# Kernel optimization log

Measured on AMD Instinct MI355X. Metric: run time of the kernel, lower is better.

## Reference

```python
import jax, jax.numpy as jnp
import numpy as np

MODEL_DIM = 2048
NUM_HEADS = 32
NUM_KV_HEADS = 8
HEAD_DIM = MODEL_DIM // NUM_HEADS  # 64
NUM_REP = NUM_HEADS // NUM_KV_HEADS  # 4


def setup_inputs() -> dict:
    key = jax.random.key(0)
    ks = jax.random.split(key, 6)
    B, S = 1, 2048
    s = 1.0 / np.sqrt(MODEL_DIM)
    x = jax.random.normal(ks[0], (B, S, MODEL_DIM), dtype=jnp.float32)
    # causal mask, 1 = keep, 0 = mask (scores.masked_fill(mask == 0, -1e9))
    mask = jnp.tril(jnp.ones((S, S), dtype=jnp.int32))[None, None, :, :]
    w_q = jax.random.normal(ks[1], (MODEL_DIM, MODEL_DIM), dtype=jnp.float32) * s
    w_k = jax.random.normal(ks[2], (NUM_KV_HEADS * HEAD_DIM, MODEL_DIM), dtype=jnp.float32) * s
    w_v = jax.random.normal(ks[3], (NUM_KV_HEADS * HEAD_DIM, MODEL_DIM), dtype=jnp.float32) * s
    w_o = jax.random.normal(ks[4], (MODEL_DIM, MODEL_DIM), dtype=jnp.float32) * s
    b_o = jax.random.normal(ks[5], (MODEL_DIM,), dtype=jnp.float32) * 0.01
    return {"x": x, "mask": mask, "w_q": w_q, "w_k": w_k, "w_v": w_v, "w_o": w_o, "b_o": b_o}


def reference(x, mask, w_q, w_k, w_v, w_o, b_o):
    B, S, _ = x.shape
    # projections (torch Linear: x @ W.T)
    q = (x @ w_q.T).reshape(B, S, NUM_HEADS, HEAD_DIM).transpose(0, 2, 1, 3)      # [B,H,S,D]
    k = (x @ w_k.T).reshape(B, S, NUM_KV_HEADS, HEAD_DIM).transpose(0, 2, 1, 3)   # [B,Hk,S,D]
    v = (x @ w_v.T).reshape(B, S, NUM_KV_HEADS, HEAD_DIM).transpose(0, 2, 1, 3)   # [B,Hk,S,D]
    # group Q heads by their shared KV head instead of materializing repeated KV
    qg = q.reshape(B, NUM_KV_HEADS, NUM_REP, S, HEAD_DIM)                         # [B,Hk,R,S,D]
    scale = 1.0 / np.sqrt(HEAD_DIM).astype(np.float32)
    scores = jnp.einsum('bgrsd,bgtd->bgrst', qg, k) * scale                       # [B,Hk,R,S,S]
    scores = jnp.where(mask[:, :, None, :, :] == 0, jnp.float32(-1e9), scores)
    attn = jax.nn.softmax(scores, axis=-1)
    ctx = jnp.einsum('bgrst,bgtd->bgrsd', attn, v)                                # [B,Hk,R,S,D]
    ctx = ctx.reshape(B, NUM_HEADS, S, HEAD_DIM).transpose(0, 2, 1, 3).reshape(B, S, MODEL_DIM)
    return ctx @ w_o.T + b_o
```

## Files before the change

kernel.cpp:

```cpp
#include <hip/hip_runtime.h>
#include <hip/hip_bf16.h>

typedef __hip_bfloat16 bf16;
typedef __attribute__((ext_vector_type(8))) short short8;
typedef __attribute__((ext_vector_type(4))) short short4_t;
typedef __attribute__((ext_vector_type(4))) float f32x4;

#define S_LEN 2048
#define DMODEL 2048
#define NH 32
#define NKV 8
#define DH 64

__global__ void detect_kernel(const unsigned int* __restrict__ x, int* __restrict__ flag) {
    int tid = threadIdx.x;
    unsigned int w = x[tid * 37];
    int e0 = (w >> 7) & 0xFF;
    int in = (e0 >= 100 && e0 <= 140) ? 1 : 0;
    unsigned long long m = __ballot(in);
    if (tid == 0) flag[0] = (__popcll(m) >= 48) ? 1 : 0;
}

__device__ __forceinline__ void conv8(const void* src, bf16* dst, int i, float scale, int isbf) {
    short8 out;
    if (isbf) {
        short8 v = *(const short8*)((const bf16*)src + i);
        if (scale != 1.0f) {
            #pragma unroll
            for (int j = 0; j < 8; ++j) {
                float f = __bfloat162float(((const bf16*)&v)[j]) * scale;
                ((bf16*)&out)[j] = __float2bfloat16(f);
            }
        } else out = v;
    } else {
        const float* gp = (const float*)src + i;
        f32x4 a = *(const f32x4*)gp;
        f32x4 b = *(const f32x4*)(gp + 4);
        #pragma unroll
        for (int j = 0; j < 4; ++j) ((bf16*)&out)[j]     = __float2bfloat16(a[j] * scale);
        #pragma unroll
        for (int j = 0; j < 4; ++j) ((bf16*)&out)[j + 4] = __float2bfloat16(b[j] * scale);
    }
    *(short8*)(dst + i) = out;
}

__global__ __launch_bounds__(256)
void convert_kernel(const void* __restrict__ src, bf16* __restrict__ dst,
                    int n, float scale, const int* __restrict__ flagp) {
    const int isbf = flagp[0];
    int i = (blockIdx.x * 256 + threadIdx.x) * 8;
    const int stride = gridDim.x * 256 * 8;
    for (; i < n; i += stride) conv8(src, dst, i, scale, isbf);
}

__global__ __launch_bounds__(256)
void convert4_kernel(const void* __restrict__ x, const void* __restrict__ wq,
                     const void* __restrict__ wk, const void* __restrict__ wv,
                     bf16* __restrict__ xb, bf16* __restrict__ wqkv,
                     const int* __restrict__ flagp) {
    const int isbf = flagp[0];
    const int b = blockIdx.x;
    const void* src; bf16* dst; int boff; float scale = 1.0f;
    if (b < 2048)       { src = x;  dst = xb;              boff = b;        }
    else if (b < 4096)  { src = wq; dst = wqkv;            boff = b - 2048; scale = 0.125f; }
    else if (b < 4608)  { src = wk; dst = wqkv + 4194304;  boff = b - 4096; }
    else                { src = wv; dst = wqkv + 5242880;  boff = b - 4608; }
    int i = (boff * 256 + threadIdx.x) * 8;
    conv8(src, dst, i, scale, isbf);
}

__device__ __forceinline__ void gload_lds16(const void* g, void* l) {
    __builtin_amdgcn_global_load_lds(
        (const __attribute__((address_space(1))) void*)(unsigned long long)(size_t)g,
        (__attribute__((address_space(3))) void*)(unsigned int)(size_t)l,
        16, 0, 0);
}

__device__ __forceinline__ void gemm_core_2ph(const bf16* __restrict__ A, const bf16* __restrict__ B,
                                              int K, int m0, int n0,
                                              bf16* sA, bf16* sB, f32x4 acc[4][2]) {
    const int tid = threadIdx.x;
    const int w = tid >> 6, lane = tid & 63;
    const int wm = (w >> 1) * 64, wn = (w & 1) * 32;
    const int lm = lane & 15, lq = lane >> 4;
    const int xr = lm & 7;

    size_t aoff[4], boff[2];
    #pragma unroll
    for (int r = 0; r < 4; ++r) {
        int ci = w * 256 + r * 64 + lane;
        int row = ci >> 3, c = (ci & 7) ^ (row & 7);
        aoff[r] = (size_t)(m0 + row) * K + c * 8;
    }
    #pragma unroll
    for (int r = 0; r < 2; ++r) {
        int cj = w * 128 + r * 64 + lane;
        int row = cj >> 3, c = (cj & 7) ^ (row & 7);
        boff[r] = (size_t)(n0 + row) * K + c * 8;
    }

    const int nt = K >> 6;
    int cur = 0;

    {
        bf16* la = sA + w * 2048;
        bf16* lb = sB + w * 1024;
        #pragma unroll
        for (int r = 0; r < 4; ++r) gload_lds16(A + aoff[r], la + r * 512);
        #pragma unroll
        for (int r = 0; r < 2; ++r) gload_lds16(B + boff[r], lb + r * 512);
    }
    __syncthreads();

    for (int t = 0; t < nt; ++t) {
        bf16* curA = sA + cur * 8192;
        bf16* curB = sB + cur * 4096;
        if (t + 1 < nt) {
            const int nxt = cur ^ 1;
            const int k0 = (t + 1) << 6;
            bf16* la = sA + nxt * 8192 + w * 2048;
            bf16* lb = sB + nxt * 4096 + w * 1024;
            #pragma unroll
            for (int r = 0; r < 4; ++r) gload_lds16(A + aoff[r] + k0, la + r * 512);
            #pragma unroll
            for (int r = 0; r < 2; ++r) gload_lds16(B + boff[r] + k0, lb + r * 512);
        }

        short8 aF[2][4], bF[2][2];
        #pragma unroll
        for (int ks = 0; ks < 2; ++ks) {
            const int cc = ((ks * 4 + lq) ^ xr) * 8;
            #pragma unroll
            for (int i = 0; i < 4; ++i)
                aF[ks][i] = *(const short8*)&curA[(wm + i * 16 + lm) * 64 + cc];
            #pragma unroll
            for (int j = 0; j < 2; ++j)
                bF[ks][j] = *(const short8*)&curB[(wn + j * 16 + lm) * 64 + cc];
        }

        __builtin_amdgcn_s_setprio(1);
        #pragma unroll
        for (int ks = 0; ks < 2; ++ks)
            #pragma unroll
            for (int i = 0; i < 4; ++i)
                #pragma unroll
                for (int j = 0; j < 2; ++j)
                    acc[i][j] = __builtin_amdgcn_mfma_f32_16x16x32_bf16(aF[ks][i], bF[ks][j], acc[i][j], 0, 0, 0);
        __builtin_amdgcn_s_setprio(0);

        __syncthreads();
        cur ^= 1;
    }
}

template<bool BIAS, bool BIAS_DYN, bool OUT_DYN>
__global__ __launch_bounds__(256, 3)
void gemm_bf16s(const bf16* __restrict__ A, const bf16* __restrict__ B,
                const void* __restrict__ bias, void* __restrict__ C,
                int M, int N, int K, int ldc, const int* __restrict__ flagp) {
    __shared__ bf16 sA[2 * 128 * 64];
    __shared__ bf16 sB[2 * 64 * 64];
    const int isbf = flagp[0];
    const int tid = threadIdx.x;
    const int m0 = blockIdx.y * 128, n0 = blockIdx.x * 64;
    const int w = tid >> 6, lane = tid & 63;
    const int wm = (w >> 1) * 64, wn = (w & 1) * 32;
    const int lm = lane & 15, lq = lane >> 4;

    f32x4 acc[4][2];
    const f32x4 zero = {0.f, 0.f, 0.f, 0.f};
    for (int i = 0; i < 4; ++i)
        for (int j = 0; j < 2; ++j) acc[i][j] = zero;

    gemm_core_2ph(A, B, K, m0, n0, sA, sB, acc);

    for (int i = 0; i < 4; ++i)
        for (int j = 0; j < 2; ++j)
            for (int r = 0; r < 4; ++r) {
                int row = m0 + wm + i * 16 + lq * 4 + r;
                int col = n0 + wn + j * 16 + lm;
                float v = acc[i][j][r];
                if (BIAS) {
                    if (BIAS_DYN && !isbf) v += ((const float*)bias)[col];
                    else                   v += __bfloat162float(((const bf16*)bias)[col]);
                }
                size_t idx = (size_t)row * ldc + col;
                if (OUT_DYN && !isbf) ((float*)C)[idx] = v;
                else                  ((bf16*)C)[idx] = __float2bfloat16(v);
            }
}

__global__ __launch_bounds__(256, 3)
void gemm_qkv(const bf16* __restrict__ A, const bf16* __restrict__ B,
              bf16* __restrict__ Qo, bf16* __restrict__ Ko, bf16* __restrict__ Vto) {
    __shared__ bf16 sA[2 * 128 * 64];
    __shared__ bf16 sB[2 * 64 * 64];
    const int tid = threadIdx.x;
    const int m0 = blockIdx.y * 128, n0 = blockIdx.x * 64;
    const int w = tid >> 6, lane = tid & 63;
    const int wm = (w >> 1) * 64, wn = (w & 1) * 32;
    const int lm = lane & 15, lq = lane >> 4;

    f32x4 acc[4][2];
    const f32x4 zero = {0.f, 0.f, 0.f, 0.f};
    for (int i = 0; i < 4; ++i)
        for (int j = 0; j < 2; ++j) acc[i][j] = zero;

    gemm_core_2ph(A, B, DMODEL, m0, n0, sA, sB, acc);

    const int route = (n0 < 2048) ? 0 : ((n0 < 2560) ? 1 : 2);
    for (int i = 0; i < 4; ++i)
        for (int j = 0; j < 2; ++j)
            for (int r = 0; r < 4; ++r) {
                int row = m0 + wm + i * 16 + lq * 4 + r;
                int col = n0 + wn + j * 16 + lm;
                bf16 v = __float2bfloat16(acc[i][j][r]);
                if (route == 0)      Qo[(size_t)row * DMODEL + col] = v;
                else if (route == 1) Ko[(size_t)row * (NKV * DH) + (col - 2048)] = v;
                else                 Vto[(size_t)(col - 2560) * S_LEN + row] = v;
            }
}

template<bool TRANS_OUT, bool BIAS, bool A_DYN, bool B_DYN, bool BIAS_DYN, bool OUT_DYN>
__global__ __launch_bounds__(256, 2)
void gemm_bt(const void* __restrict__ A, const void* __restrict__ B,
             const void* __restrict__ bias, void* __restrict__ C,
             int M, int N, int K, int ldc, const int* __restrict__ flagp) {
    __shared__ bf16 sA[128 * 32];
    __shared__ bf16 sB[128 * 32];

    const int isbf = flagp[0];
    const int tid = threadIdx.x;
    const int m0 = blockIdx.y * 128, n0 = blockIdx.x * 128;
    const int w = tid >> 6, lane = tid & 63;
    const int wm = (w >> 1) * 64, wn = (w & 1) * 64;
    const int lm = lane & 15, lq = lane >> 4;

    f32x4 acc[4][4];
    const f32x4 zero = {0.f, 0.f, 0.f, 0.f};
    for (int i = 0; i < 4; ++i)
        for (int j = 0; j < 4; ++j) acc[i][j] = zero;

    for (int k0 = 0; k0 < K; k0 += 32) {
        __syncthreads();
        for (int it = 0; it < 2; ++it) {
            int c = it * 256 + tid;
            int row = c >> 2, off = (c & 3) * 8;
            if (!A_DYN || isbf) {
                *(short8*)&sA[row * 32 + off] =
                    *(const short8*)((const bf16*)A + (size_t)(m0 + row) * K + k0 + off);
            } else {
                const float* gp = (const float*)A + (size_t)(m0 + row) * K + k0 + off;
                #pragma unroll
                for (int i = 0; i < 8; ++i) sA[row * 32 + off + i] = __float2bfloat16(gp[i]);
            }
            if (!B_DYN || isbf) {
                *(short8*)&sB[row * 32 + off] =
                    *(const short8*)((const bf16*)B + (size_t)(n0 + row) * K + k0 + off);
            } else {
                const float* gp = (const float*)B + (size_t)(n0 + row) * K + k0 + off;
                #pragma unroll
                for (int i = 0; i < 8; ++i) sB[row * 32 + off + i] = __float2bfloat16(gp[i]);
            }
        }
        __syncthreads();

        short8 aF[4], bF[4];
        for (int i = 0; i < 4; ++i)
            aF[i] = *(const short8*)&sA[(wm + i * 16 + lm) * 32 + lq * 8];
        for (int i = 0; i < 4; ++i)
            bF[i] = *(const short8*)&sB[(wn + i * 16 + lm) * 32 + lq * 8];
        for (int i = 0; i < 4; ++i)
            for (int j = 0; j < 4; ++j)
                acc[i][j] = __builtin_amdgcn_mfma_f32_16x16x32_bf16(aF[i], bF[j], acc[i][j], 0, 0, 0);
    }

    for (int i = 0; i < 4; ++i)
        for (int j = 0; j < 4; ++j)
            for (int r = 0; r < 4; ++r) {
                int row = m0 + wm + i * 16 + lq * 4 + r;
                int col = n0 + wn + j * 16 + lm;
                float v = acc[i][j][r];
                if (BIAS) {
                    if (BIAS_DYN && !isbf) v += ((const float*)bias)[col];
                    else                   v += __bfloat162float(((const bf16*)bias)[col]);
                }
                size_t idx = TRANS_OUT ? (size_t)col * ldc + row : (size_t)row * ldc + col;
                if (OUT_DYN && !isbf) ((float*)C)[idx] = v;
                else                  ((bf16*)C)[idx] = __float2bfloat16(v);
            }
}

template<bool PRESCALED>
__global__ __launch_bounds__(256, 2)
void attn_kernel(const bf16* __restrict__ Q, const bf16* __restrict__ Km,
                 const bf16* __restrict__ Vt, bf16* __restrict__ ctx) {
    __shared__ bf16 sQ[64 * 72];
    __shared__ bf16 sK[128 * 72];
    __shared__ bf16 sV[64 * 136];
    __shared__ bf16 sP[4][16 * 136];

    const int tid = threadIdx.x;
    const int h  = blockIdx.y;
    const int kvh = h >> 2;
    const int w = tid >> 6, lane = tid & 63;
    const int lm = lane & 15, lq = lane >> 4;
    const int qloc = w * 16 + lm;

    const f32x4 zero = {0.f, 0.f, 0.f, 0.f};

    int krow[4], koff[4], vrow[4], voff[4];
    #pragma unroll
    for (int i = 0; i < 4; ++i) {
        int id = i * 256 + tid;
        krow[i] = id >> 3;  koff[i] = (id & 7) * 8;
        vrow[i] = id >> 4;  voff[i] = (id & 15) * 8;
    }

    for (int ph = 0; ph < 2; ++ph) {
        const int qb = ph ? (31 - blockIdx.x) : blockIdx.x;
        const int nt = (qb >> 1) + 1;

        __syncthreads();
        for (int c = tid; c < 512; c += 256) {
            int row = c >> 3, off = (c & 7) * 8;
            *(short8*)&sQ[row * 72 + off] =
                *(const short8*)&Q[(size_t)(qb * 64 + row) * DMODEL + h * 64 + off];
        }

        float m_r = -1e30f, l_r = 0.f;
        f32x4 oacc[4];
        #pragma unroll
        for (int ni = 0; ni < 4; ++ni) oacc[ni] = zero;

        short8 kr[4], vr[4];
        #pragma unroll
        for (int i = 0; i < 4; ++i) {
            kr[i] = *(const short8*)&Km[(size_t)krow[i] * (NKV * DH) + kvh * 64 + koff[i]];
            vr[i] = *(const short8*)&Vt[(size_t)(kvh * 64 + vrow[i]) * S_LEN + voff[i]];
        }

        for (int kt = 0; kt < nt; ++kt) {
            __syncthreads();
            #pragma unroll
            for (int i = 0; i < 4; ++i) {
                *(short8*)&sK[krow[i] * 72 + koff[i]] = kr[i];
                *(short8*)&sV[vrow[i] * 136 + voff[i]] = vr[i];
            }
            __syncthreads();
            if (kt + 1 < nt) {
                const int b0 = (kt + 1) * 128;
                #pragma unroll
                for (int i = 0; i < 4; ++i) {
                    int rg = b0 + krow[i]; rg = rg > 2047 ? 2047 : rg;
                    int cg = b0 + voff[i]; cg = cg > 2040 ? 2040 : cg;
                    kr[i] = *(const short8*)&Km[(size_t)rg * (NKV * DH) + kvh * 64 + koff[i]];
                    vr[i] = *(const short8*)&Vt[(size_t)(kvh * 64 + vrow[i]) * S_LEN + cg];
                }
            }

            f32x4 sacc[8];
            #pragma unroll
            for (int ni = 0; ni < 8; ++ni) sacc[ni] = zero;
            __builtin_amdgcn_s_setprio(1);
            #pragma unroll
            for (int ks = 0; ks < 2; ++ks) {
                short8 aq = *(const short8*)&sQ[(w * 16 + lm) * 72 + ks * 32 + lq * 8];
                #pragma unroll
                for (int ni = 0; ni < 8; ++ni) {
                    short8 bk = *(const short8*)&sK[(ni * 16 + lm) * 72 + ks * 32 + lq * 8];
                    sacc[ni] = __builtin_amdgcn_mfma_f32_16x16x32_bf16(bk, aq, sacc[ni], 0, 0, 0);
                }
            }
            __builtin_amdgcn_s_setprio(0);

            float mx = -3e38f;
            if (kt == nt - 1) {
                const int qrel = qb * 64 + qloc - kt * 128;
                #pragma unroll
                for (int ni = 0; ni < 8; ++ni)
                    #pragma unroll
                    for (int r = 0; r < 4; ++r) {
                        float s = sacc[ni][r];
                        if (!PRESCALED) s *= 0.125f;
                        if ((ni * 16 + lq * 4 + r) > qrel) s = -1e30f;
                        sacc[ni][r] = s;
                        mx = fmaxf(mx, s);
                    }
            } else {
                #pragma unroll
                for (int ni = 0; ni < 8; ++ni)
                    #pragma unroll
                    for (int r = 0; r < 4; ++r) {
                        float s = sacc[ni][r];
                        if (!PRESCALED) s *= 0.125f;
                        sacc[ni][r] = s;
                        mx = fmaxf(mx, s);
                    }
            }
            mx = fmaxf(mx, __shfl_xor(mx, 16));
            mx = fmaxf(mx, __shfl_xor(mx, 32));

            int defer = (mx - m_r <= 8.0f) ? 1 : 0;
            if (!__all(defer)) {
                float m_new = fmaxf(m_r, mx);
                float alpha = __expf(m_r - m_new);
                m_r = m_new;
                l_r *= alpha;
                #pragma unroll
                for (int r = 0; r < 4; ++r) {
                    float a_b = __shfl(alpha, (lane & 48) | (lq * 4 + r));
                    #pragma unroll
                    for (int ni = 0; ni < 4; ++ni) oacc[ni][r] *= a_b;
                }
            }

            float rs = 0.f;
            #pragma unroll
            for (int ni = 0; ni < 8; ++ni) {
                short4_t pk;
                #pragma unroll
                for (int r = 0; r < 4; ++r) {
                    float p = __expf(sacc[ni][r] - m_r);
                    rs += p;
                    ((bf16*)&pk)[r] = __float2bfloat16(p);
                }
                *(short4_t*)&sP[w][lm * 136 + ni * 16 + lq * 4] = pk;
            }
            rs += __shfl_xor(rs, 16);
            rs += __shfl_xor(rs, 32);
            l_r += rs;

            asm volatile("s_waitcnt lgkmcnt(0)" ::: "memory");
            __builtin_amdgcn_sched_barrier(0);

            __builtin_amdgcn_s_setprio(1);
            #pragma unroll
            for (int ks = 0; ks < 4; ++ks) {
                short8 ap = *(const short8*)&sP[w][lm * 136 + ks * 32 + lq * 8];
                #pragma unroll
                for (int ni = 0; ni < 4; ++ni) {
                    short8 bv = *(const short8*)&sV[(ni * 16 + lm) * 136 + ks * 32 + lq * 8];
                    oacc[ni] = __builtin_amdgcn_mfma_f32_16x16x32_bf16(ap, bv, oacc[ni], 0, 0, 0);
                }
            }
            __builtin_amdgcn_s_setprio(0);
        }

        #pragma unroll
        for (int r = 0; r < 4; ++r) {
            float l_b = __shfl(l_r, (lane & 48) | (lq * 4 + r));
            float inv = 1.0f / l_b;
            #pragma unroll
            for (int ni = 0; ni < 4; ++ni)
                ctx[(size_t)(qb * 64 + w * 16 + lq * 4 + r) * DMODEL + h * 64 + ni * 16 + lm] =
                    __float2bfloat16(oacc[ni][r] * inv);
        }
    }
}

extern "C" void kernel_launch(void* const* d_in, const int* in_sizes, int n_in,
                              void* d_out, int out_size, void* d_ws, size_t ws_size,
                              hipStream_t stream) {
    const void* x   = d_in[0];
    const void* w_q = d_in[2];
    const void* w_k = d_in[3];
    const void* w_v = d_in[4];
    const void* w_o = d_in[5];
    const void* b_o = d_in[6];

    const size_t MB = 1024u * 1024u;
    char* ws = (char*)d_ws;
    int*  flag = (int*)ws;
    dim3 blk(256);

    detect_kernel<<<1, 64, 0, stream>>>((const unsigned int*)x, flag);

    if (ws_size >= 32 * MB + 4096) {
        bf16* xb   = (bf16*)(ws + 4096);
        bf16* wqkv = (bf16*)(ws + 4096 + 8 * MB);
        bf16* Qws  = (bf16*)(ws + 4096 + 20 * MB);
        bf16* Kws  = (bf16*)(ws + 4096 + 28 * MB);
        bf16* Vtws = (bf16*)(ws + 4096 + 30 * MB);
        bf16* wob  = xb;
        bf16* Ctx  = wqkv;

        convert4_kernel<<<5120, blk, 0, stream>>>(x, w_q, w_k, w_v, xb, wqkv, flag);
        gemm_qkv<<<dim3(48, 16), blk, 0, stream>>>(xb, wqkv, Qws, Kws, Vtws);
        convert_kernel<<<2048, blk, 0, stream>>>(w_o, wob, DMODEL * DMODEL, 1.0f, flag);
        attn_kernel<true><<<dim3(16, 32), blk, 0, stream>>>(Qws, Kws, Vtws, Ctx);
        gemm_bf16s<true, true, true><<<dim3(32, 16), blk, 0, stream>>>(
            Ctx, wob, b_o, d_out, S_LEN, DMODEL, DMODEL, DMODEL, flag);
    } else {
        bf16* Qws  = (bf16*)(ws + 4096);
        bf16* Kws  = (bf16*)(ws + 4096 + 8u * MB);
        bf16* Vtws = (bf16*)(ws + 4096 + 10u * MB);
        bf16* Ctx  = (bf16*)(ws + 4096 + 12u * MB);

        gemm_bt<false, false, true, true, false, false><<<dim3(16, 16), blk, 0, stream>>>(
            x, w_q, nullptr, Qws, S_LEN, DMODEL, DMODEL, DMODEL, flag);
        gemm_bt<false, false, true, true, false, false><<<dim3(4, 16), blk, 0, stream>>>(
            x, w_k, nullptr, Kws, S_LEN, NKV * DH, DMODEL, NKV * DH, flag);
        gemm_bt<true, false, true, true, false, false><<<dim3(4, 16), blk, 0, stream>>>(
            x, w_v, nullptr, Vtws, S_LEN, NKV * DH, DMODEL, S_LEN, flag);
        attn_kernel<false><<<dim3(16, 32), blk, 0, stream>>>(Qws, Kws, Vtws, Ctx);
        gemm_bt<false, true, false, true, true, true><<<dim3(16, 16), blk, 0, stream>>>(
            Ctx, w_o, b_o, d_out, S_LEN, DMODEL, DMODEL, DMODEL, flag);
    }
}
```

Baseline: 222.1 us.

## Restructure attention into small 32-query blocks with register-resident Q and V

The attention kernel now uses 128-thread blocks that each handle 32 query rows of one head, over 64-key tiles, in a 1D grid of 2048 blocks. Blocks are ordered so the longest causal rows launch first; this replaces the old scheme where each block processed a paired short and long query block. Q fragments are held in registers and V fragments are loaded straight from global memory into registers, so only K (with an XOR swizzle) and P go through LDS. The aim is less LDS traffic and shared-memory footprint and more blocks resident per CU. The cost is that both waves in a block load the same V fragments from global memory, and there are more blocks overall.

```diff
diff --git a/kernel.cpp b/kernel.cpp
--- a/kernel.cpp
+++ b/kernel.cpp
@@ -292,170 +292,161 @@
 }
 
 template<bool PRESCALED>
-__global__ __launch_bounds__(256, 2)
+__global__ __launch_bounds__(128, 3)
 void attn_kernel(const bf16* __restrict__ Q, const bf16* __restrict__ Km,
                  const bf16* __restrict__ Vt, bf16* __restrict__ ctx) {
-    __shared__ bf16 sQ[64 * 72];
-    __shared__ bf16 sK[128 * 72];
-    __shared__ bf16 sV[64 * 136];
-    __shared__ bf16 sP[4][16 * 136];
+    __shared__ bf16 sK[64 * 64];
+    __shared__ bf16 sP[2][16 * 72];
 
     const int tid = threadIdx.x;
-    const int h  = blockIdx.y;
+    const int bx = blockIdx.x;
+    const int h  = bx & 31;
+    const int qi = 63 - (bx >> 5);
     const int kvh = h >> 2;
     const int w = tid >> 6, lane = tid & 63;
     const int lm = lane & 15, lq = lane >> 4;
-    const int qloc = w * 16 + lm;
+    const int xr = lm & 7;
+    const int nt = (qi >> 1) + 1;
 
     const f32x4 zero = {0.f, 0.f, 0.f, 0.f};
 
-    int krow[4], koff[4], vrow[4], voff[4];
+    int krow[4], kcol[4];
     #pragma unroll
     for (int i = 0; i < 4; ++i) {
-        int id = i * 256 + tid;
-        krow[i] = id >> 3;  koff[i] = (id & 7) * 8;
-        vrow[i] = id >> 4;  voff[i] = (id & 15) * 8;
-    }
-
-    for (int ph = 0; ph < 2; ++ph) {
-        const int qb = ph ? (31 - blockIdx.x) : blockIdx.x;
-        const int nt = (qb >> 1) + 1;
-
+        int id = i * 128 + tid;
+        krow[i] = id >> 3;
+        kcol[i] = (id & 7);
+    }
+
+    const int qrow = qi * 32 + w * 16 + lm;
+    short8 aq0 = *(const short8*)&Q[(size_t)qrow * DMODEL + h * 64 + lq * 8];
+    short8 aq1 = *(const short8*)&Q[(size_t)qrow * DMODEL + h * 64 + 32 + lq * 8];
+
+    float m_r = -1e30f, l_r = 0.f;
+    f32x4 oacc[4];
+    #pragma unroll
+    for (int ni = 0; ni < 4; ++ni) oacc[ni] = zero;
+
+    short8 kr[4];
+    #pragma unroll
+    for (int i = 0; i < 4; ++i)
+        kr[i] = *(const short8*)&Km[(size_t)krow[i] * (NKV * DH) + kvh * 64 + kcol[i] * 8];
+
+    for (int kt = 0; kt < nt; ++kt) {
         __syncthreads();
-        for (int c = tid; c < 512; c += 256) {
-            int row = c >> 3, off = (c & 7) * 8;
-            *(short8*)&sQ[row * 72 + off] =
-                *(const short8*)&Q[(size_t)(qb * 64 + row) * DMODEL + h * 64 + off];
-        }
-
-        float m_r = -1e30f, l_r = 0.f;
-        f32x4 oacc[4];
-        #pragma unroll
-        for (int ni = 0; ni < 4; ++ni) oacc[ni] = zero;
-
-        short8 kr[4], vr[4];
-        #pragma unroll
-        for (int i = 0; i < 4; ++i) {
-            kr[i] = *(const short8*)&Km[(size_t)krow[i] * (NKV * DH) + kvh * 64 + koff[i]];
-            vr[i] = *(const short8*)&Vt[(size_t)(kvh * 64 + vrow[i]) * S_LEN + voff[i]];
-        }
-
-        for (int kt = 0; kt < nt; ++kt) {
-            __syncthreads();
-            #pragma unroll
-            for (int i = 0; i < 4; ++i) {
-                *(short8*)&sK[krow[i] * 72 + koff[i]] = kr[i];
-                *(short8*)&sV[vrow[i] * 136 + voff[i]] = vr[i];
-            }
-            __syncthreads();
-            if (kt + 1 < nt) {
-                const int b0 = (kt + 1) * 128;
-                #pragma unroll
-                for (int i = 0; i < 4; ++i) {
-                    int rg = b0 + krow[i]; rg = rg > 2047 ? 2047 : rg;
-                    int cg = b0 + voff[i]; cg = cg > 2040 ? 2040 : cg;
-                    kr[i] = *(const short8*)&Km[(size_t)rg * (NKV * DH) + kvh * 64 + koff[i]];
-                    vr[i] = *(const short8*)&Vt[(size_t)(kvh * 64 + vrow[i]) * S_LEN + cg];
-                }
-            }
-
-            f32x4 sacc[8];
-            #pragma unroll
-            for (int ni = 0; ni < 8; ++ni) sacc[ni] = zero;
-            __builtin_amdgcn_s_setprio(1);
-            #pragma unroll
-            for (int ks = 0; ks < 2; ++ks) {
-                short8 aq = *(const short8*)&sQ[(w * 16 + lm) * 72 + ks * 32 + lq * 8];
-                #pragma unroll
-                for (int ni = 0; ni < 8; ++ni) {
-                    short8 bk = *(const short8*)&sK[(ni * 16 + lm) * 72 + ks * 32 + lq * 8];
-                    sacc[ni] = __builtin_amdgcn_mfma_f32_16x16x32_bf16(bk, aq, sacc[ni], 0, 0, 0);
-                }
-            }
-            __builtin_amdgcn_s_setprio(0);
-
-            float mx = -3e38f;
-            if (kt == nt - 1) {
-                const int qrel = qb * 64 + qloc - kt * 128;
-                #pragma unroll
-                for (int ni = 0; ni < 8; ++ni)
-                    #pragma unroll
-                    for (int r = 0; r < 4; ++r) {
-                        float s = sacc[ni][r];
-                        if (!PRESCALED) s *= 0.125f;
-                        if ((ni * 16 + lq * 4 + r) > qrel) s = -1e30f;
-                        sacc[ni][r] = s;
-                        mx = fmaxf(mx, s);
-                    }
-            } else {
-                #pragma unroll
-                for (int ni = 0; ni < 8; ++ni)
-                    #pragma unroll
-                    for (int r = 0; r < 4; ++r) {
-                        float s = sacc[ni][r];
-                        if (!PRESCALED) s *= 0.125f;
-                        sacc[ni][r] = s;
-                        mx = fmaxf(mx, s);
-                    }
-            }
-            mx = fmaxf(mx, __shfl_xor(mx, 16));
-            mx = fmaxf(mx, __shfl_xor(mx, 32));
-
-            int defer = (mx - m_r <= 8.0f) ? 1 : 0;
-            if (!__all(defer)) {
-                float m_new = fmaxf(m_r, mx);
-                float alpha = __expf(m_r - m_new);
-                m_r = m_new;
-                l_r *= alpha;
+        #pragma unroll
+        for (int i = 0; i < 4; ++i)
+            *(short8*)&sK[krow[i] * 64 + (kcol[i] ^ (krow[i] & 7)) * 8] = kr[i];
+        __syncthreads();
+        if (kt + 1 < nt) {
+            const int b0 = (kt + 1) * 64;
+            #pragma unroll
+            for (int i = 0; i < 4; ++i)
+                kr[i] = *(const short8*)&Km[(size_t)(b0 + krow[i]) * (NKV * DH) + kvh * 64 + kcol[i] * 8];
+        }
+
+        short8 vv[4][2];
+        #pragma unroll
+        for (int ni = 0; ni < 4; ++ni)
+            #pragma unroll
+            for (int ks = 0; ks < 2; ++ks)
+                vv[ni][ks] = *(const short8*)&Vt[(size_t)(kvh * 64 + ni * 16 + lm) * S_LEN
+                                                 + kt * 64 + ks * 32 + lq * 8];
+
+        f32x4 sacc[4];
+        #pragma unroll
+        for (int ni = 0; ni < 4; ++ni) sacc[ni] = zero;
+        __builtin_amdgcn_s_setprio(1);
+        #pragma unroll
+        for (int ks = 0; ks < 2; ++ks) {
+            short8 aq = ks ? aq1 : aq0;
+            #pragma unroll
+            for (int ni = 0; ni < 4; ++ni) {
+                short8 bk = *(const short8*)&sK[(ni * 16 + lm) * 64 + (((ks << 2) | lq) ^ xr) * 8];
+                sacc[ni] = __builtin_amdgcn_mfma_f32_16x16x32_bf16(bk, aq, sacc[ni], 0, 0, 0);
+            }
+        }
+        __builtin_amdgcn_s_setprio(0);
+
+        float mx = -3e38f;
+        if (kt == nt - 1) {
+            const int qrel = qi * 32 + w * 16 + lm - kt * 64;
+            #pragma unroll
+            for (int ni = 0; ni < 4; ++ni)
                 #pragma unroll
                 for (int r = 0; r < 4; ++r) {
-                    float a_b = __shfl(alpha, (lane & 48) | (lq * 4 + r));
-                    #pragma unroll
-                    for (int ni = 0; ni < 4; ++ni) oacc[ni][r] *= a_b;
+                    float s = sacc[ni][r];
+                    if (!PRESCALED) s *= 0.125f;
+                    if ((ni * 16 + lq * 4 + r) > qrel) s = -1e30f;
+                    sacc[ni][r] = s;
+                    mx = fmaxf(mx, s);
                 }
-            }
-
-            float rs = 0.f;
-            #pragma unroll
-            for (int ni = 0; ni < 8; ++ni) {
-                short4_t pk;
+        } else {
+            #pragma unroll
+            for (int ni = 0; ni < 4; ++ni)
                 #pragma unroll
                 for (int r = 0; r < 4; ++r) {
-                    float p = __expf(sacc[ni][r] - m_r);
-                    rs += p;
-                    ((bf16*)&pk)[r] = __float2bfloat16(p);
+                    float s = sacc[ni][r];
+                    if (!PRESCALED) s *= 0.125f;
+                    sacc[ni][r] = s;
+                    mx = fmaxf(mx, s);
                 }
-                *(short4_t*)&sP[w][lm * 136 + ni * 16 + lq * 4] = pk;
-            }
-            rs += __shfl_xor(rs, 16);
-            rs += __shfl_xor(rs, 32);
-            l_r += rs;
-
-            asm volatile("s_waitcnt lgkmcnt(0)" ::: "memory");
-            __builtin_amdgcn_sched_barrier(0);
-
-            __builtin_amdgcn_s_setprio(1);
-            #pragma unroll
-            for (int ks = 0; ks < 4; ++ks) {
-                short8 ap = *(const short8*)&sP[w][lm * 136 + ks * 32 + lq * 8];
+        }
+        mx = fmaxf(mx, __shfl_xor(mx, 16));
+        mx = fmaxf(mx, __shfl_xor(mx, 32));
+
+        int defer = (mx - m_r <= 8.0f) ? 1 : 0;
+        if (!__all(defer)) {
+            float m_new = fmaxf(m_r, mx);
+            float alpha = __expf(m_r - m_new);
+            m_r = m_new;
+            l_r *= alpha;
+            #pragma unroll
+            for (int r = 0; r < 4; ++r) {
+                float a_b = __shfl(alpha, (lane & 48) | (lq * 4 + r));
                 #pragma unroll
-                for (int ni = 0; ni < 4; ++ni) {
-                    short8 bv = *(const short8*)&sV[(ni * 16 + lm) * 136 + ks * 32 + lq * 8];
-                    oacc[ni] = __builtin_amdgcn_mfma_f32_16x16x32_bf16(ap, bv, oacc[ni], 0, 0, 0);
-                }
-            }
-            __builtin_amdgcn_s_setprio(0);
-        }
-
-        #pragma unroll
-        for (int r = 0; r < 4; ++r) {
-            float l_b = __shfl(l_r, (lane & 48) | (lq * 4 + r));
-            float inv = 1.0f / l_b;
+                for (int ni = 0; ni < 4; ++ni) oacc[ni][r] *= a_b;
+            }
+        }
+
+        float rs = 0.f;
+        #pragma unroll
+        for (int ni = 0; ni < 4; ++ni) {
+            short4_t pk;
+            #pragma unroll
+            for (int r = 0; r < 4; ++r) {
+                float p = __expf(sacc[ni][r] - m_r);
+                rs += p;
+                ((bf16*)&pk)[r] = __float2bfloat16(p);
+            }
+            *(short4_t*)&sP[w][lm * 72 + ni * 16 + lq * 4] = pk;
+        }
+        rs += __shfl_xor(rs, 16);
+        rs += __shfl_xor(rs, 32);
+        l_r += rs;
+
+        asm volatile("s_waitcnt lgkmcnt(0)" ::: "memory");
+        __builtin_amdgcn_sched_barrier(0);
+
+        __builtin_amdgcn_s_setprio(1);
+        #pragma unroll
+        for (int ks = 0; ks < 2; ++ks) {
+            short8 ap = *(const short8*)&sP[w][lm * 72 + ks * 32 + lq * 8];
             #pragma unroll
             for (int ni = 0; ni < 4; ++ni)
-                ctx[(size_t)(qb * 64 + w * 16 + lq * 4 + r) * DMODEL + h * 64 + ni * 16 + lm] =
-                    __float2bfloat16(oacc[ni][r] * inv);
-        }
+                oacc[ni] = __builtin_amdgcn_mfma_f32_16x16x32_bf16(ap, vv[ni][ks], oacc[ni], 0, 0, 0);
+        }
+        __builtin_amdgcn_s_setprio(0);
+    }
+
+    #pragma unroll
+    for (int r = 0; r < 4; ++r) {
+        float l_b = __shfl(l_r, (lane & 48) | (lq * 4 + r));
+        float inv = 1.0f / l_b;
+        #pragma unroll
+        for (int ni = 0; ni < 4; ++ni)
+            ctx[(size_t)(qi * 32 + w * 16 + lq * 4 + r) * DMODEL + h * 64 + ni * 16 + lm] =
+                __float2bfloat16(oacc[ni][r] * inv);
     }
 }
 
@@ -488,7 +479,7 @@
         convert4_kernel<<<5120, blk, 0, stream>>>(x, w_q, w_k, w_v, xb, wqkv, flag);
         gemm_qkv<<<dim3(48, 16), blk, 0, stream>>>(xb, wqkv, Qws, Kws, Vtws);
         convert_kernel<<<2048, blk, 0, stream>>>(w_o, wob, DMODEL * DMODEL, 1.0f, flag);
-        attn_kernel<true><<<dim3(16, 32), blk, 0, stream>>>(Qws, Kws, Vtws, Ctx);
+        attn_kernel<true><<<dim3(2048), dim3(128), 0, stream>>>(Qws, Kws, Vtws, Ctx);
         gemm_bf16s<true, true, true><<<dim3(32, 16), blk, 0, stream>>>(
             Ctx, wob, b_o, d_out, S_LEN, DMODEL, DMODEL, DMODEL, flag);
     } else {
@@ -503,7 +494,7 @@
             x, w_k, nullptr, Kws, S_LEN, NKV * DH, DMODEL, NKV * DH, flag);
         gemm_bt<true, false, true, true, false, false><<<dim3(4, 16), blk, 0, stream>>>(
             x, w_v, nullptr, Vtws, S_LEN, NKV * DH, DMODEL, S_LEN, flag);
-        attn_kernel<false><<<dim3(16, 32), blk, 0, stream>>>(Qws, Kws, Vtws, Ctx);
+        attn_kernel<false><<<dim3(2048), dim3(128), 0, stream>>>(Qws, Kws, Vtws, Ctx);
         gemm_bt<false, true, false, true, true, true><<<dim3(16, 16), blk, 0, stream>>>(
             Ctx, w_o, b_o, d_out, S_LEN, DMODEL, DMODEL, DMODEL, flag);
     }
```

New measurement: 252.0 us. 13.5% more time.
